# Kernel optimization log

Hardware: AMD Instinct MI355X
Metric: run time of the kernel (lower is better)

## Reference

```python
import jax, jax.numpy as jnp
import numpy as np


def _normalize_adj(edge_index, num_nodes):
    # add self loops
    loop = jnp.arange(num_nodes, dtype=edge_index.dtype)
    row = jnp.concatenate([edge_index[0], loop])
    col = jnp.concatenate([edge_index[1], loop])
    deg = jax.ops.segment_sum(jnp.ones(row.shape[0], jnp.float32), row,
                              num_segments=num_nodes)
    dis = jnp.where(deg > 0, jax.lax.rsqrt(deg), 0.0)  # deg^{-1/2}, inf->0
    ew = dis[row] * dis[col]
    return row, col, ew


def _gcn_conv(x, W, b, row, col, ew, num_nodes):
    h = x @ W.T + b                       # dense linear [N, out]
    msg = h[col] * ew[:, None]            # gather + scale [E', out]
    return jax.ops.segment_sum(msg, row, num_segments=num_nodes)  # scatter_add


def setup_inputs() -> dict:
    N, E, IN, HID, OUT = 100000, 1600000, 128, 128, 64
    key = jax.random.key(0)
    k1, k2, k3, k4 = jax.random.split(key, 4)
    x = jax.random.normal(k1, (N, IN), jnp.float32)
    edge_index = jax.random.randint(k2, (2, E), 0, N, jnp.int64)
    # xavier_uniform for weights, zero bias (as in reset_parameters)
    lim1 = float(np.sqrt(6.0 / (IN + HID)))
    lim2 = float(np.sqrt(6.0 / (HID + OUT)))
    W1 = jax.random.uniform(k3, (HID, IN), jnp.float32, -lim1, lim1)
    b1 = jnp.zeros((HID,), jnp.float32)
    W2 = jax.random.uniform(k4, (OUT, HID), jnp.float32, -lim2, lim2)
    b2 = jnp.zeros((OUT,), jnp.float32)
    return {"x": x, "edge_index": edge_index, "num_nodes": N,
            "W1": W1, "b1": b1, "W2": W2, "b2": b2}


def reference(x, edge_index, num_nodes, W1, b1, W2, b2):
    row, col, ew = _normalize_adj(edge_index, num_nodes)
    h = _gcn_conv(x, W1, b1, row, col, ew, num_nodes)
    h = jax.nn.relu(h)  # dropout is identity in eval mode
    out = _gcn_conv(h, W2, b2, row, col, ew, num_nodes)
    return out
```

## Files before the change

### kernel.cpp

```cpp
#include <hip/hip_runtime.h>
#include <hip/hip_bf16.h>
#include <stdint.h>


#define TPB 256
#define NBLK_C 256
#define TPB_C 1024
#define MAX_NB 2048

typedef __attribute__((ext_vector_type(8))) __bf16 bf16x8;
typedef __attribute__((ext_vector_type(4))) float f32x4;
typedef __attribute__((ext_vector_type(2))) float f32x2;

__device__ __forceinline__ float bf16lo(unsigned u) { return __uint_as_float(u << 16); }
__device__ __forceinline__ float bf16hi(unsigned u) { return __uint_as_float(u & 0xffff0000u); }
__device__ __forceinline__ unsigned short f2bf(float f) {
    unsigned u = __float_as_uint(f);
    return (unsigned short)((u + 0x7fff + ((u >> 16) & 1)) >> 16);
}
__device__ __forceinline__ f32x2 pk_add(f32x2 a, f32x2 b) {
    f32x2 d;
    asm("v_pk_add_f32 %0, %1, %2" : "=v"(d) : "v"(a), "v"(b));
    return d;
}

__global__ __launch_bounds__(TPB_C) void hist_extract_kernel(const void* __restrict__ ei, int E,
                                                             int CH,
                                                             int* __restrict__ row32,
                                                             int* __restrict__ col32,
                                                             int* __restrict__ hist,
                                                             int NB, int N) {
    __shared__ int h[MAX_NB];
    __shared__ int s_is64;
    int tid = threadIdx.x;
    if (tid < 64) {
        int x = ((const int*)ei)[2 * tid + 1];
        unsigned long long b = __ballot(x != 0);
        if (tid == 0) s_is64 = (b == 0ull);
    }
    for (int bin = tid; bin < NB; bin += TPB_C) h[bin] = 0;
    __syncthreads();

    int b = blockIdx.x;
    int s = b * CH;
    int end = min(E, s + CH);
    int is64 = s_is64;
    unsigned uN = (unsigned)N;
    if (is64) {
        const long long* p = (const long long*)ei;
        for (int e = s + tid; e < end; e += TPB_C) {
            int r = (int)p[e];
            int c = (int)p[E + e];
            row32[e] = r;
            col32[e] = c;
            if ((unsigned)r < uN && (unsigned)c < uN) atomicAdd(&h[r >> 7], 1);
        }
    } else {
        const int* p = (const int*)ei;
        for (int e = s + tid; e < end; e += TPB_C) {
            int r = p[e];
            int c = p[E + e];
            row32[e] = r;
            col32[e] = c;
            if ((unsigned)r < uN && (unsigned)c < uN) atomicAdd(&h[r >> 7], 1);
        }
    }
    __syncthreads();
    for (int bin = tid; bin < NB; bin += TPB_C) hist[bin * NBLK_C + b] = h[bin];
}

__global__ __launch_bounds__(NBLK_C) void colscan_kernel(int* __restrict__ hist,
                                                         int* __restrict__ binTotal) {
    __shared__ int sm[NBLK_C];
    int bin = blockIdx.x;
    int tid = threadIdx.x;
    int v = hist[bin * NBLK_C + tid];
    sm[tid] = v;
    __syncthreads();
    for (int o = 1; o < NBLK_C; o <<= 1) {
        int x = (tid >= o) ? sm[tid - o] : 0;
        __syncthreads();
        sm[tid] += x;
        __syncthreads();
    }
    hist[bin * NBLK_C + tid] = sm[tid] - v;
    if (tid == NBLK_C - 1) binTotal[bin] = sm[NBLK_C - 1];
}

__global__ __launch_bounds__(TPB_C) void scatter_kernel(const int* __restrict__ row32,
                                                        const int* __restrict__ col32, int E,
                                                        int CH,
                                                        const int* __restrict__ hist,
                                                        const int* __restrict__ binTotal,
                                                        int* __restrict__ bucketed,
                                                        int NB, int N) {
    __shared__ int cur[MAX_NB];
    __shared__ int sm2[TPB_C];
    int tid = threadIdx.x;
    int b = blockIdx.x;

    int v = (tid < NB) ? binTotal[tid] : 0;
    sm2[tid] = v;
    __syncthreads();
    for (int o = 1; o < TPB_C; o <<= 1) {
        int x = (tid >= o) ? sm2[tid - o] : 0;
        __syncthreads();
        sm2[tid] += x;
        __syncthreads();
    }
    if (tid < NB) cur[tid] = (sm2[tid] - v) + hist[tid * NBLK_C + b];
    __syncthreads();

    int s = b * CH;
    int end = min(E, s + CH);
    unsigned uN = (unsigned)N;
    for (int e = s + tid; e < end; e += TPB_C) {
        int r = row32[e];
        int c = col32[e];
        if ((unsigned)r < uN && (unsigned)c < uN) {
            int pos = atomicAdd(&cur[r >> 7], 1);
            bucketed[pos] = (c << 7) | (r & 127);
        }
    }
}

__global__ __launch_bounds__(TPB) void finecsr_kernel(const int* __restrict__ bucketed,
                                                      const int* __restrict__ binTotal,
                                                      int* __restrict__ offs,
                                                      int* __restrict__ cnt,
                                                      float* __restrict__ dis,
                                                      int* __restrict__ csr, int N) {
    __shared__ int c128[128];
    __shared__ int cur128[128];
    __shared__ int sm[TPB];
    __shared__ int red[TPB];
    int bin = blockIdx.x;
    int tid = threadIdx.x;

    int part = 0;
    for (int i = tid; i < bin; i += TPB) part += binTotal[i];
    red[tid] = part;
    __syncthreads();
    for (int o = TPB / 2; o > 0; o >>= 1) {
        if (tid < o) red[tid] += red[tid + o];
        __syncthreads();
    }
    int s = red[0];
    int m = binTotal[bin];

    if (tid < 128) c128[tid] = 0;
    __syncthreads();
    for (int i = tid; i < m; i += TPB) atomicAdd(&c128[bucketed[s + i] & 127], 1);
    __syncthreads();

    int v = (tid < 128) ? c128[tid] : 0;
    sm[tid] = v;
    __syncthreads();
    for (int o = 1; o < 128; o <<= 1) {
        int x = (tid >= o) ? sm[tid - o] : 0;
        __syncthreads();
        sm[tid] += x;
        __syncthreads();
    }
    if (tid < 128) {
        int excl = sm[tid] - v;
        int r = bin * 128 + tid;
        if (r < N) {
            offs[r] = s + excl;
            cnt[r] = v;
            dis[r] = rsqrtf((float)v + 1.0f);
        }
        cur128[tid] = s + excl;
    }
    __syncthreads();
    for (int i = tid; i < m; i += TPB) {
        int p = bucketed[s + i];
        int pos = atomicAdd(&cur128[p & 127], 1);
        csr[pos] = p >> 7;
    }
}

template <int BN, bool INB16>
__global__ __launch_bounds__(256, 2) void gemm_mfma_kernel(const void* __restrict__ Xp,
                                                           const float* __restrict__ W,
                                                           const float* __restrict__ bias,
                                                           const float* __restrict__ dis,
                                                           unsigned short* __restrict__ Hb,
                                                           int N) {
    constexpr int XST = 136;
    __shared__ unsigned short Xs[128 * XST];
    __shared__ unsigned short Ws[BN * XST];

    const int tid = threadIdx.x;
    const int r0 = blockIdx.x * 128;

    if (blockIdx.x == 0 && tid < (BN >> 1))
        ((unsigned*)Hb)[(size_t)N * (BN >> 1) + tid] = 0u;

    if (INB16) {
        const ushort4* Xv = (const ushort4*)Xp;
        for (int idx = tid; idx < 128 * 32; idx += 256) {
            int row = idx >> 5, q = idx & 31;
            int rg = r0 + row;
            if (rg >= N) rg = N - 1;
            *(ushort4*)&Xs[row * XST + q * 4] = Xv[(size_t)rg * 32 + q];
        }
    } else {
        const float4* Xv = (const float4*)Xp;
        for (int idx = tid; idx < 128 * 32; idx += 256) {
            int row = idx >> 5, q = idx & 31;
            int rg = r0 + row;
            if (rg >= N) rg = N - 1;
            float4 v = Xv[(size_t)rg * 32 + q];
            ushort4 s = make_ushort4(f2bf(v.x), f2bf(v.y), f2bf(v.z), f2bf(v.w));
            *(ushort4*)&Xs[row * XST + q * 4] = s;
        }
    }
    {
        const float4* Wv = (const float4*)W;
        for (int idx = tid; idx < BN * 32; idx += 256) {
            int n = idx >> 5, q = idx & 31;
            float4 v = Wv[n * 32 + q];
            ushort4 s = make_ushort4(f2bf(v.x), f2bf(v.y), f2bf(v.z), f2bf(v.w));
            *(ushort4*)&Ws[n * XST + q * 4] = s;
        }
    }
    __syncthreads();

    constexpr int RT = (BN == 128) ? 4 : 2;
    constexpr int CT = 4;
    const int wave = tid >> 6, lane = tid & 63;
    const int l15 = lane & 15, q8 = lane >> 4;
    const int row0 = (BN == 128) ? (wave & 1) * 64 : wave * 32;
    const int col0 = (BN == 128) ? (wave >> 1) * 64 : 0;

    f32x4 zero = {0.f, 0.f, 0.f, 0.f};
    f32x4 acc[RT][CT];
#pragma unroll
    for (int rt = 0; rt < RT; ++rt)
#pragma unroll
        for (int ct = 0; ct < CT; ++ct) acc[rt][ct] = zero;

#pragma unroll
    for (int ks = 0; ks < 4; ++ks) {
        int ko = ks * 32 + q8 * 8;
        bf16x8 a[RT], b[CT];
#pragma unroll
        for (int rt = 0; rt < RT; ++rt)
            a[rt] = *(const bf16x8*)&Xs[(row0 + rt * 16 + l15) * XST + ko];
#pragma unroll
        for (int ct = 0; ct < CT; ++ct)
            b[ct] = *(const bf16x8*)&Ws[(col0 + ct * 16 + l15) * XST + ko];
#pragma unroll
        for (int rt = 0; rt < RT; ++rt)
#pragma unroll
            for (int ct = 0; ct < CT; ++ct)
                acc[rt][ct] = __builtin_amdgcn_mfma_f32_16x16x32_bf16(
                    a[rt], b[ct], acc[rt][ct], 0, 0, 0);
    }

    float bv[CT];
#pragma unroll
    for (int ct = 0; ct < CT; ++ct) bv[ct] = bias[col0 + ct * 16 + l15];
#pragma unroll
    for (int rt = 0; rt < RT; ++rt)
#pragma unroll
        for (int r = 0; r < 4; ++r) {
            int row = r0 + row0 + rt * 16 + q8 * 4 + r;
            if (row < N) {
                float dn = dis[row];
#pragma unroll
                for (int ct = 0; ct < CT; ++ct)
                    Hb[(size_t)row * BN + col0 + ct * 16 + l15] =
                        f2bf((acc[rt][ct][r] + bv[ct]) * dn);
            }
        }
}

template <int F, bool RELU, bool OB16>
__global__ __launch_bounds__(TPB) void agg_kernel(const unsigned short* __restrict__ Hb,
                                                  const int* __restrict__ csr,
                                                  const int* __restrict__ offs,
                                                  const int* __restrict__ cnt,
                                                  const float* __restrict__ dis,
                                                  void* __restrict__ outp, int N) {
    constexpr int FPL = F / 16;
    constexpr int NW = FPL / 2;
    constexpr int RS = F / 2;

    int w = (blockIdx.x * TPB + threadIdx.x) >> 6;
    if (w >= N) return;
    int lane = threadIdx.x & 63;
    int g = lane >> 4;
    int fl = lane & 15;

    float di = dis[w];
    int s = offs[w];
    int d = cnt[w];

    const unsigned* Hu = (const unsigned*)Hb;

    f32x2 acc2[NW];
#pragma unroll
    for (int t = 0; t < NW; ++t) acc2[t] = (f32x2){0.f, 0.f};

    auto accum_row = [&](const unsigned (&u)[NW]) {
#pragma unroll
        for (int t = 0; t < NW; ++t) {
            f32x2 lh;
            lh.x = bf16lo(u[t]);
            lh.y = bf16hi(u[t]);
            acc2[t] = pk_add(acc2[t], lh);
        }
    };
    auto load_row = [&](unsigned (&u)[NW], int r) {
        if constexpr (NW == 4) {
            uint4 v = *(const uint4*)(Hu + (size_t)r * RS + fl * NW);
            u[0] = v.x; u[1] = v.y; u[2] = v.z; u[3] = v.w;
        } else {
            uint2 v = *(const uint2*)(Hu + (size_t)r * RS + fl * NW);
            u[0] = v.x; u[1] = v.y;
        }
    };

    if (g == 0) {
        unsigned su[NW];
        load_row(su, w);
        accum_row(su);
    }

    for (int base = 0; base < d; base += 64) {
        int rem = d - base;
        if (rem > 64) rem = 64;
        int cl = (lane < rem) ? csr[s + base + lane] : 0;

        for (int e = 0; e < rem; e += 32) {
            int cc0[4];
#pragma unroll
            for (int k = 0; k < 4; ++k) {
                int idx = e + k * 4 + g;
                int raw = __shfl(cl, idx & 63);
                cc0[k] = (idx < rem) ? raw : N;
            }
            unsigned u0[4][NW];
#pragma unroll
            for (int k = 0; k < 4; ++k) load_row(u0[k], cc0[k]);

            const bool two = (e + 16) < rem;
            int cc1[4];
            unsigned u1[4][NW];
            if (two) {
#pragma unroll
                for (int k = 0; k < 4; ++k) {
                    int idx = e + 16 + k * 4 + g;
                    int raw = __shfl(cl, idx & 63);
                    cc1[k] = (idx < rem) ? raw : N;
                }
#pragma unroll
                for (int k = 0; k < 4; ++k) load_row(u1[k], cc1[k]);
            }
#pragma unroll
            for (int k = 0; k < 4; ++k) accum_row(u0[k]);
            if (two) {
#pragma unroll
                for (int k = 0; k < 4; ++k) accum_row(u1[k]);
            }
        }
    }

#pragma unroll
    for (int off = 16; off < 64; off <<= 1)
#pragma unroll
        for (int t = 0; t < NW; ++t) {
            acc2[t].x += __shfl_xor(acc2[t].x, off);
            acc2[t].y += __shfl_xor(acc2[t].y, off);
        }

#pragma unroll
    for (int t = 0; t < NW; ++t) {
        acc2[t].x *= di;
        acc2[t].y *= di;
        if (RELU) {
            acc2[t].x = fmaxf(acc2[t].x, 0.0f);
            acc2[t].y = fmaxf(acc2[t].y, 0.0f);
        }
    }

    if (lane < 16) {
        if constexpr (OB16) {
            unsigned dw[NW];
#pragma unroll
            for (int t = 0; t < NW; ++t)
                dw[t] = (unsigned)f2bf(acc2[t].x) | ((unsigned)f2bf(acc2[t].y) << 16);
            unsigned* op = (unsigned*)outp;
            if constexpr (NW == 4) {
                *(uint4*)&op[(size_t)w * RS + fl * NW] = make_uint4(dw[0], dw[1], dw[2], dw[3]);
            } else {
                *(uint2*)&op[(size_t)w * RS + fl * NW] = make_uint2(dw[0], dw[1]);
            }
        } else {
            float4* op = (float4*)outp;
            if constexpr (NW == 2) {
                op[(size_t)w * 16 + fl] =
                    make_float4(acc2[0].x, acc2[0].y, acc2[1].x, acc2[1].y);
            } else {
                op[(size_t)w * 32 + fl * 2] =
                    make_float4(acc2[0].x, acc2[0].y, acc2[1].x, acc2[1].y);
                op[(size_t)w * 32 + fl * 2 + 1] =
                    make_float4(acc2[2].x, acc2[2].y, acc2[3].x, acc2[3].y);
            }
        }
    }
}

extern "C" void kernel_launch(void* const* d_in, const int* in_sizes, int n_in,
                              void* d_out, int out_size, void* d_ws, size_t ws_size,
                              hipStream_t stream) {
    const float* x  = (const float*)d_in[0];
    const void*  ei = d_in[1];
    const float* W1 = (const float*)d_in[3];
    const float* b1 = (const float*)d_in[4];
    const float* W2 = (const float*)d_in[5];
    const float* b2 = (const float*)d_in[6];
    float* out = (float*)d_out;

    const int IN = 128, HID = 128;
    const int N = in_sizes[0] / IN;
    const int E = in_sizes[1] / 2;
    const int NB = (N + 127) >> 7;
    const int CH = (E + NBLK_C - 1) / NBLK_C;

    char* ws = (char*)d_ws;
    size_t off = 0;
    auto alloc = [&](size_t bytes) -> void* {
        void* p = (void*)(ws + off);
        off += (bytes + 255) & ~(size_t)255;
        return p;
    };
    int*   cnt      = (int*)alloc((size_t)N * 4);
    int*   offs     = (int*)alloc((size_t)N * 4);
    float* dis      = (float*)alloc((size_t)N * 4);
    int*   row32    = (int*)alloc((size_t)E * 4);
    int*   col32    = (int*)alloc((size_t)E * 4);
    int*   bucketed = (int*)alloc((size_t)E * 4);
    int*   csr      = (int*)alloc((size_t)E * 4);
    int*   hist     = (int*)alloc((size_t)NB * NBLK_C * 4);
    int*   binTotal = (int*)alloc((size_t)NB * 4);
    unsigned short* H1b = (unsigned short*)alloc((size_t)(N + 1) * HID * 2);
    unsigned short* R1b = (unsigned short*)alloc((size_t)(N + 1) * HID * 2);
    unsigned short* H2b = H1b;

    hist_extract_kernel<<<NBLK_C, TPB_C, 0, stream>>>(ei, E, CH, row32, col32,
                                                      hist, NB, N);
    colscan_kernel<<<NB, NBLK_C, 0, stream>>>(hist, binTotal);
    scatter_kernel<<<NBLK_C, TPB_C, 0, stream>>>(row32, col32, E, CH, hist, binTotal,
                                                 bucketed, NB, N);
    finecsr_kernel<<<NB, TPB, 0, stream>>>(bucketed, binTotal, offs, cnt, dis, csr, N);

    int ngrid = (N + 127) / 128;

    gemm_mfma_kernel<128, false><<<ngrid, 256, 0, stream>>>(x, W1, b1, dis, H1b, N);
    agg_kernel<128, true, true><<<(N + 3) / 4, TPB, 0, stream>>>(H1b, csr, offs, cnt,
                                                                 dis, R1b, N);

    gemm_mfma_kernel<64, true><<<ngrid, 256, 0, stream>>>(R1b, W2, b2, dis, H2b, N);
    agg_kernel<64, false, false><<<(N + 3) / 4, TPB, 0, stream>>>(H2b, csr, offs, cnt,
                                                                  dis, out, N);
}
```

Baseline: 274.3 us.

## Use persistent grid-stride aggregation with prefetched node metadata and packed int4 meta

Aggregation kernels now launch a capped grid of 2048 blocks. Each wave walks nodes with a grid stride and prefetches the next node's offset, degree, norm and first 64 neighbour indices while processing the current node. Offset, count and norm are packed into one int4 per node, so a single load replaces three. The aim is to hide the dependent metadata and CSR load latency and to cut launch cost per wave. The risk is lower parallelism, since 2048 blocks of 4 waves may not fill the GPU as well as one wave per node did, and the persistent loop adds register pressure.

```diff
diff --git a/kernel.cpp b/kernel.cpp
--- a/kernel.cpp
+++ b/kernel.cpp
@@ -126,8 +126,7 @@
 
 __global__ __launch_bounds__(TPB) void finecsr_kernel(const int* __restrict__ bucketed,
                                                       const int* __restrict__ binTotal,
-                                                      int* __restrict__ offs,
-                                                      int* __restrict__ cnt,
+                                                      int4* __restrict__ meta,
                                                       float* __restrict__ dis,
                                                       int* __restrict__ csr, int N) {
     __shared__ int c128[128];
@@ -166,9 +165,9 @@
         int excl = sm[tid] - v;
         int r = bin * 128 + tid;
         if (r < N) {
-            offs[r] = s + excl;
-            cnt[r] = v;
-            dis[r] = rsqrtf((float)v + 1.0f);
+            float dv = rsqrtf((float)v + 1.0f);
+            meta[r] = make_int4(s + excl, v, __float_as_int(dv), 0);
+            dis[r] = dv;
         }
         cur128[tid] = s + excl;
     }
@@ -280,39 +279,22 @@
 template <int F, bool RELU, bool OB16>
 __global__ __launch_bounds__(TPB) void agg_kernel(const unsigned short* __restrict__ Hb,
                                                   const int* __restrict__ csr,
-                                                  const int* __restrict__ offs,
-                                                  const int* __restrict__ cnt,
-                                                  const float* __restrict__ dis,
+                                                  const int4* __restrict__ meta,
                                                   void* __restrict__ outp, int N) {
     constexpr int FPL = F / 16;
     constexpr int NW = FPL / 2;
     constexpr int RS = F / 2;
 
-    int w = (blockIdx.x * TPB + threadIdx.x) >> 6;
+    const int lane = threadIdx.x & 63;
+    const int g = lane >> 4;
+    const int fl = lane & 15;
+    const int W = gridDim.x << 2;
+
+    int w = (blockIdx.x << 2) + (threadIdx.x >> 6);
     if (w >= N) return;
-    int lane = threadIdx.x & 63;
-    int g = lane >> 4;
-    int fl = lane & 15;
-
-    float di = dis[w];
-    int s = offs[w];
-    int d = cnt[w];
 
     const unsigned* Hu = (const unsigned*)Hb;
 
-    f32x2 acc2[NW];
-#pragma unroll
-    for (int t = 0; t < NW; ++t) acc2[t] = (f32x2){0.f, 0.f};
-
-    auto accum_row = [&](const unsigned (&u)[NW]) {
-#pragma unroll
-        for (int t = 0; t < NW; ++t) {
-            f32x2 lh;
-            lh.x = bf16lo(u[t]);
-            lh.y = bf16hi(u[t]);
-            acc2[t] = pk_add(acc2[t], lh);
-        }
-    };
     auto load_row = [&](unsigned (&u)[NW], int r) {
         if constexpr (NW == 4) {
             uint4 v = *(const uint4*)(Hu + (size_t)r * RS + fl * NW);
@@ -323,93 +305,129 @@
         }
     };
 
-    if (g == 0) {
-        unsigned su[NW];
-        load_row(su, w);
-        accum_row(su);
-    }
-
-    for (int base = 0; base < d; base += 64) {
-        int rem = d - base;
-        if (rem > 64) rem = 64;
-        int cl = (lane < rem) ? csr[s + base + lane] : 0;
-
-        for (int e = 0; e < rem; e += 32) {
-            int cc0[4];
-#pragma unroll
-            for (int k = 0; k < 4; ++k) {
-                int idx = e + k * 4 + g;
-                int raw = __shfl(cl, idx & 63);
-                cc0[k] = (idx < rem) ? raw : N;
-            }
-            unsigned u0[4][NW];
-#pragma unroll
-            for (int k = 0; k < 4; ++k) load_row(u0[k], cc0[k]);
-
-            const bool two = (e + 16) < rem;
-            int cc1[4];
-            unsigned u1[4][NW];
-            if (two) {
+    int4 m = meta[w];
+    int s = m.x, d = m.y;
+    float di = __int_as_float(m.z);
+    int cl = (lane < d) ? csr[s + lane] : 0;
+
+    while (true) {
+        const int wn = w + W;
+        const bool has_next = wn < N;
+        int sn = 0, dn = 0, cln = 0;
+        float din = 0.f;
+        if (has_next) {
+            int4 mn = meta[wn];
+            sn = mn.x; dn = mn.y; din = __int_as_float(mn.z);
+            cln = (lane < dn) ? csr[sn + lane] : 0;
+        }
+
+        f32x2 acc2[NW];
+#pragma unroll
+        for (int t = 0; t < NW; ++t) acc2[t] = (f32x2){0.f, 0.f};
+
+        auto accum_row = [&](const unsigned (&u)[NW]) {
+#pragma unroll
+            for (int t = 0; t < NW; ++t) {
+                f32x2 lh;
+                lh.x = bf16lo(u[t]);
+                lh.y = bf16hi(u[t]);
+                acc2[t] = pk_add(acc2[t], lh);
+            }
+        };
+
+        if (g == 0) {
+            unsigned su[NW];
+            load_row(su, w);
+            accum_row(su);
+        }
+
+        int clc = cl;
+        for (int base = 0; base < d; base += 64) {
+            int rem = d - base;
+            if (rem > 64) rem = 64;
+            if (base > 0) clc = (lane < rem) ? csr[s + base + lane] : 0;
+
+            for (int e = 0; e < rem; e += 32) {
+                int cc0[4];
 #pragma unroll
                 for (int k = 0; k < 4; ++k) {
-                    int idx = e + 16 + k * 4 + g;
-                    int raw = __shfl(cl, idx & 63);
-                    cc1[k] = (idx < rem) ? raw : N;
+                    int idx = e + k * 4 + g;
+                    int raw = __shfl(clc, idx & 63);
+                    cc0[k] = (idx < rem) ? raw : N;
                 }
-#pragma unroll
-                for (int k = 0; k < 4; ++k) load_row(u1[k], cc1[k]);
-            }
-#pragma unroll
-            for (int k = 0; k < 4; ++k) accum_row(u0[k]);
-            if (two) {
-#pragma unroll
-                for (int k = 0; k < 4; ++k) accum_row(u1[k]);
-            }
-        }
-    }
-
-#pragma unroll
-    for (int off = 16; off < 64; off <<= 1)
+                unsigned u0[4][NW];
+#pragma unroll
+                for (int k = 0; k < 4; ++k) load_row(u0[k], cc0[k]);
+
+                const bool two = (e + 16) < rem;
+                int cc1[4];
+                unsigned u1[4][NW];
+                if (two) {
+#pragma unroll
+                    for (int k = 0; k < 4; ++k) {
+                        int idx = e + 16 + k * 4 + g;
+                        int raw = __shfl(clc, idx & 63);
+                        cc1[k] = (idx < rem) ? raw : N;
+                    }
+#pragma unroll
+                    for (int k = 0; k < 4; ++k) load_row(u1[k], cc1[k]);
+                }
+#pragma unroll
+                for (int k = 0; k < 4; ++k) accum_row(u0[k]);
+                if (two) {
+#pragma unroll
+                    for (int k = 0; k < 4; ++k) accum_row(u1[k]);
+                }
+            }
+        }
+
+#pragma unroll
+        for (int off = 16; off < 64; off <<= 1)
+#pragma unroll
+            for (int t = 0; t < NW; ++t) {
+                acc2[t].x += __shfl_xor(acc2[t].x, off);
+                acc2[t].y += __shfl_xor(acc2[t].y, off);
+            }
+
 #pragma unroll
         for (int t = 0; t < NW; ++t) {
-            acc2[t].x += __shfl_xor(acc2[t].x, off);
-            acc2[t].y += __shfl_xor(acc2[t].y, off);
-        }
-
-#pragma unroll
-    for (int t = 0; t < NW; ++t) {
-        acc2[t].x *= di;
-        acc2[t].y *= di;
-        if (RELU) {
-            acc2[t].x = fmaxf(acc2[t].x, 0.0f);
-            acc2[t].y = fmaxf(acc2[t].y, 0.0f);
-        }
-    }
-
-    if (lane < 16) {
-        if constexpr (OB16) {
-            unsigned dw[NW];
-#pragma unroll
-            for (int t = 0; t < NW; ++t)
-                dw[t] = (unsigned)f2bf(acc2[t].x) | ((unsigned)f2bf(acc2[t].y) << 16);
-            unsigned* op = (unsigned*)outp;
-            if constexpr (NW == 4) {
-                *(uint4*)&op[(size_t)w * RS + fl * NW] = make_uint4(dw[0], dw[1], dw[2], dw[3]);
+            acc2[t].x *= di;
+            acc2[t].y *= di;
+            if (RELU) {
+                acc2[t].x = fmaxf(acc2[t].x, 0.0f);
+                acc2[t].y = fmaxf(acc2[t].y, 0.0f);
+            }
+        }
+
+        if (lane < 16) {
+            if constexpr (OB16) {
+                unsigned dw[NW];
+#pragma unroll
+                for (int t = 0; t < NW; ++t)
+                    dw[t] = (unsigned)f2bf(acc2[t].x) | ((unsigned)f2bf(acc2[t].y) << 16);
+                unsigned* op = (unsigned*)outp;
+                if constexpr (NW == 4) {
+                    *(uint4*)&op[(size_t)w * RS + fl * NW] =
+                        make_uint4(dw[0], dw[1], dw[2], dw[3]);
+                } else {
+                    *(uint2*)&op[(size_t)w * RS + fl * NW] = make_uint2(dw[0], dw[1]);
+                }
             } else {
-                *(uint2*)&op[(size_t)w * RS + fl * NW] = make_uint2(dw[0], dw[1]);
-            }
-        } else {
-            float4* op = (float4*)outp;
-            if constexpr (NW == 2) {
-                op[(size_t)w * 16 + fl] =
-                    make_float4(acc2[0].x, acc2[0].y, acc2[1].x, acc2[1].y);
-            } else {
-                op[(size_t)w * 32 + fl * 2] =
-                    make_float4(acc2[0].x, acc2[0].y, acc2[1].x, acc2[1].y);
-                op[(size_t)w * 32 + fl * 2 + 1] =
-                    make_float4(acc2[2].x, acc2[2].y, acc2[3].x, acc2[3].y);
-            }
-        }
+                float4* op = (float4*)outp;
+                if constexpr (NW == 2) {
+                    op[(size_t)w * 16 + fl] =
+                        make_float4(acc2[0].x, acc2[0].y, acc2[1].x, acc2[1].y);
+                } else {
+                    op[(size_t)w * 32 + fl * 2] =
+                        make_float4(acc2[0].x, acc2[0].y, acc2[1].x, acc2[1].y);
+                    op[(size_t)w * 32 + fl * 2 + 1] =
+                        make_float4(acc2[2].x, acc2[2].y, acc2[3].x, acc2[3].y);
+                }
+            }
+        }
+
+        if (!has_next) break;
+        w = wn; s = sn; d = dn; di = din; cl = cln;
     }
 }
 
@@ -437,8 +455,7 @@
         off += (bytes + 255) & ~(size_t)255;
         return p;
     };
-    int*   cnt      = (int*)alloc((size_t)N * 4);
-    int*   offs     = (int*)alloc((size_t)N * 4);
+    int4*  meta     = (int4*)alloc((size_t)N * 16);
     float* dis      = (float*)alloc((size_t)N * 4);
     int*   row32    = (int*)alloc((size_t)E * 4);
     int*   col32    = (int*)alloc((size_t)E * 4);
@@ -455,15 +472,15 @@
     colscan_kernel<<<NB, NBLK_C, 0, stream>>>(hist, binTotal);
     scatter_kernel<<<NBLK_C, TPB_C, 0, stream>>>(row32, col32, E, CH, hist, binTotal,
                                                  bucketed, NB, N);
-    finecsr_kernel<<<NB, TPB, 0, stream>>>(bucketed, binTotal, offs, cnt, dis, csr, N);
+    finecsr_kernel<<<NB, TPB, 0, stream>>>(bucketed, binTotal, meta, dis, csr, N);
 
     int ngrid = (N + 127) / 128;
+    int agrid = (N + 3) / 4;
+    if (agrid > 2048) agrid = 2048;
 
     gemm_mfma_kernel<128, false><<<ngrid, 256, 0, stream>>>(x, W1, b1, dis, H1b, N);
-    agg_kernel<128, true, true><<<(N + 3) / 4, TPB, 0, stream>>>(H1b, csr, offs, cnt,
-                                                                 dis, R1b, N);
+    agg_kernel<128, true, true><<<agrid, TPB, 0, stream>>>(H1b, csr, meta, R1b, N);
 
     gemm_mfma_kernel<64, true><<<ngrid, 256, 0, stream>>>(R1b, W2, b2, dis, H2b, N);
-    agg_kernel<64, false, false><<<(N + 3) / 4, TPB, 0, stream>>>(H2b, csr, offs, cnt,
-                                                                  dis, out, N);
-}
+    agg_kernel<64, false, false><<<agrid, TPB, 0, stream>>>(H2b, csr, meta, out, N);
+}
```

Result: slower. 291.1 us (+6.1%).
